# Performance work log

Hardware: AMD Instinct MI355X
Metric: run time of the kernel (lower is better)

The kernel has to match this reference:

```python
import jax, jax.numpy as jnp
import numpy as np

B, T, H, C = 256, 784, 512, 10
TRUNC = 100


def setup_inputs() -> dict:
    key = jax.random.key(0)
    ks = jax.random.split(key, 11)
    s_in = 1.0  # xavier-ish scales
    def init(k, shape, fan_in):
        return jax.random.normal(k, shape, dtype=jnp.float32) * (1.0 / np.sqrt(fan_in))
    return {
        "x": jax.random.normal(ks[0], (B, T), dtype=jnp.float32),
        "W_ih1": init(ks[1], (4 * H, 1), 1),
        "W_hh1": init(ks[2], (4 * H, H), H),
        "b_ih1": jnp.zeros((4 * H,), dtype=jnp.float32),
        "b_hh1": jnp.zeros((4 * H,), dtype=jnp.float32),
        "W_ih2": init(ks[3], (4 * H, H), H),
        "W_hh2": init(ks[4], (4 * H, H), H),
        "b_ih2": jnp.zeros((4 * H,), dtype=jnp.float32),
        "b_hh2": jnp.zeros((4 * H,), dtype=jnp.float32),
        "W_fc": init(ks[5], (C, H), H),
        "b_fc": jnp.zeros((C,), dtype=jnp.float32),
    }


def _lstm_cell(pre, h, c, W_hh, b_hh):
    # pre: input projection [B,4H]; PyTorch LSTMCell gate order: i, f, g, o
    gates = pre + h @ W_hh.T + b_hh
    i, f, g, o = jnp.split(gates, 4, axis=-1)
    c_new = jax.nn.sigmoid(f) * c + jax.nn.sigmoid(i) * jnp.tanh(g)
    h_new = jax.nn.sigmoid(o) * jnp.tanh(c_new)
    return h_new, c_new


def _forward(x, W_ih1, W_hh1, b_ih1, b_hh1, W_ih2, W_hh2, b_ih2, b_hh2, W_fc, b_fc):
    # Precompute input projections for layer 1 across all timesteps: x is scalar per step.
    # pre1_all: [T, B, 4H]
    pre1_all = x.T[:, :, None] * W_ih1[:, 0][None, None, :] + b_ih1
    t_idx = jnp.arange(T)

    def step(carry, xs):
        h1, c1, h2, c2 = carry
        pre1, t = xs
        # truncation point (detach) is identity in forward; kept for structure
        stop = (t % TRUNC) == 0
        sg = lambda a: jnp.where(stop, jax.lax.stop_gradient(a), a)
        h1, c1, h2, c2 = sg(h1), sg(c1), sg(h2), sg(c2)
        h1, c1 = _lstm_cell(pre1, h1, c1, W_hh1, b_hh1)
        pre2 = c1 @ W_ih2.T + b_ih2  # layer 2 consumes layer-1 CELL state
        h2, c2 = _lstm_cell(pre2, h2, c2, W_hh2, b_hh2)
        return (h1, c1, h2, c2), h2

    z = jnp.zeros((B, H), dtype=x.dtype)
    _, outs = jax.lax.scan(step, (z, z, z, z), (pre1_all, t_idx))  # outs: [T,B,H]
    outs = outs.transpose(1, 0, 2)  # [B,T,H]
    out = outs @ W_fc.T + b_fc  # [B,T,C]
    return out


def reference(x, W_ih1, W_hh1, b_ih1, b_hh1, W_ih2, W_hh2, b_ih2, b_hh2, W_fc, b_fc):
    return _forward(x, W_ih1, W_hh1, b_ih1, b_hh1, W_ih2, W_hh2, b_ih2, b_hh2, W_fc, b_fc)
```

## Files before the change

### kernel.cpp

```cpp
#include <hip/hip_runtime.h>


constexpr int Bn = 256;
constexpr int Tn = 784;
constexpr int Hn = 512;
constexpr int Cn = 10;

typedef short s16x8 __attribute__((ext_vector_type(8)));
typedef float f32x4 __attribute__((ext_vector_type(4)));

__device__ __forceinline__ unsigned short f2bf(float f) {
  unsigned u = __float_as_uint(f);
  u += 0x7FFFu + ((u >> 16) & 1u);
  return (unsigned short)(u >> 16);
}
__device__ __forceinline__ float bf2f(unsigned short s) {
  return __uint_as_float(((unsigned)s) << 16);
}
__device__ __forceinline__ float sigm(float v) { return 1.f / (1.f + __expf(-v)); }
__device__ __forceinline__ float tanh_(float v) {
  float vc = fminf(fmaxf(v, -15.f), 15.f);
  float e = __expf(2.f * vc);
  return (e - 1.f) / (e + 1.f);
}

__device__ __forceinline__ s16x8 load16_l2(const unsigned short* p) {
  s16x8 r;
  asm volatile("global_load_dwordx4 %0, %1, off sc0"
               : "=v"(r) : "v"(p) : "memory");
  return r;
}
__device__ __forceinline__ void load16x16_l2(const unsigned short* p, s16x8* f) {
  asm volatile(
      "global_load_dwordx4 %0, %16, off sc0\n\t"
      "global_load_dwordx4 %1, %16, off offset:64 sc0\n\t"
      "global_load_dwordx4 %2, %16, off offset:128 sc0\n\t"
      "global_load_dwordx4 %3, %16, off offset:192 sc0\n\t"
      "global_load_dwordx4 %4, %16, off offset:256 sc0\n\t"
      "global_load_dwordx4 %5, %16, off offset:320 sc0\n\t"
      "global_load_dwordx4 %6, %16, off offset:384 sc0\n\t"
      "global_load_dwordx4 %7, %16, off offset:448 sc0\n\t"
      "global_load_dwordx4 %8, %16, off offset:512 sc0\n\t"
      "global_load_dwordx4 %9, %16, off offset:576 sc0\n\t"
      "global_load_dwordx4 %10, %16, off offset:640 sc0\n\t"
      "global_load_dwordx4 %11, %16, off offset:704 sc0\n\t"
      "global_load_dwordx4 %12, %16, off offset:768 sc0\n\t"
      "global_load_dwordx4 %13, %16, off offset:832 sc0\n\t"
      "global_load_dwordx4 %14, %16, off offset:896 sc0\n\t"
      "global_load_dwordx4 %15, %16, off offset:960 sc0"
      : "=&v"(f[0]), "=&v"(f[1]), "=&v"(f[2]), "=&v"(f[3]),
        "=&v"(f[4]), "=&v"(f[5]), "=&v"(f[6]), "=&v"(f[7]),
        "=&v"(f[8]), "=&v"(f[9]), "=&v"(f[10]), "=&v"(f[11]),
        "=&v"(f[12]), "=&v"(f[13]), "=&v"(f[14]), "=&v"(f[15])
      : "v"(p) : "memory");
}
__device__ __forceinline__ void store4_l2(unsigned short* p, unsigned v0,
                                          unsigned v1, unsigned v2, unsigned v3) {
  asm volatile(
      "global_store_short %0, %1, off\n\t"
      "global_store_short %0, %2, off offset:1024\n\t"
      "global_store_short %0, %3, off offset:2048\n\t"
      "global_store_short %0, %4, off offset:3072"
      :: "v"(p), "v"(v0), "v"(v1), "v"(v2), "v"(v3) : "memory");
}
__device__ __forceinline__ void vm0_fence() {
  asm volatile("s_waitcnt vmcnt(0)" ::: "memory");
  __builtin_amdgcn_sched_barrier(0);
}
__device__ __forceinline__ unsigned ld_flag_mall(const unsigned* p) {
  unsigned r;
  asm volatile("global_load_dword %0, %1, off sc0 sc1\n\ts_waitcnt vmcnt(0)"
               : "=v"(r) : "v"(p) : "memory");
  return r;
}
__device__ __forceinline__ void st_flag_mall(unsigned* p, unsigned v) {
  asm volatile("global_store_dword %0, %1, off sc0 sc1"
               :: "v"(p), "v"(v) : "memory");
}

__device__ __forceinline__ void stage_w(char* smem, const float* W0,
                                        int js, int tid, int base) {
  for (int idx = tid * 4; idx < 64 * 512; idx += 1024) {
    int row = idx >> 9, kk = idx & 511;
    int n = ((row >> 4) << 9) + js + (row & 15);
    float4 w = *(const float4*)(W0 + (size_t)n * Hn + kk);
    short4 v = { (short)f2bf(w.x), (short)f2bf(w.y), (short)f2bf(w.z), (short)f2bf(w.w) };
    int byte = base + (row << 10) + ((((kk >> 3) ^ (row & 7)) << 4)) + ((kk & 7) << 1);
    *(short4*)(smem + byte) = v;
  }
}

__global__ void __launch_bounds__(256, 1)
lstm2_kernel(const float* __restrict__ x,
             const float* __restrict__ W_ih1, const float* __restrict__ W_hh1,
             const float* __restrict__ b_ih1, const float* __restrict__ b_hh1,
             const float* __restrict__ W_ih2, const float* __restrict__ W_hh2,
             const float* __restrict__ b_ih2, const float* __restrict__ b_hh2,
             const float* __restrict__ W_fc, const float* __restrict__ b_fc,
             float* __restrict__ out,
             unsigned* __restrict__ cnts,
             unsigned short* __restrict__ h1b,
             unsigned short* __restrict__ c1b,
             unsigned short* __restrict__ h2b)
{
  extern __shared__ char smem[];
  const int tid = threadIdx.x;
  const int wv = tid >> 6;
  const int l = tid & 63;

  if (tid == 0) {
    unsigned xcc;
    asm volatile("s_getreg_b32 %0, hwreg(HW_REG_XCC_ID)" : "=s"(xcc));
    xcc &= 7u;
    unsigned rk = atomicAdd(&cnts[512 + xcc * 16], 1u);
    *(unsigned*)(smem + 131064) = xcc;
    *(unsigned*)(smem + 131060) = rk;
  }
  __syncthreads();
  const int s8   = (int)*(const unsigned*)(smem + 131064);
  const int rank = (int)(*(const unsigned*)(smem + 131060) & 31u);
  const int rb = s8 << 5;
  const int js = rank << 4;

  unsigned* fbase = cnts + 1024 + s8 * 32;
  unsigned* myflag = fbase + rank;

  const int rA = l & 15, lg = l >> 4, lx = l & 7;
  const bool isW1 = (wv < 2);

  s16x8 bw[64];
  stage_w(smem, W_hh1, js, tid, 0);
  __syncthreads();
  if (isW1) {
#pragma unroll
    for (int g = 0; g < 4; ++g)
#pragma unroll
      for (int kc = 0; kc < 16; ++kc)
        bw[(g << 4) + kc] =
            *(const s16x8*)(smem + (((g << 4) + rA) << 10) + ((((kc << 2) + lg) ^ lx) << 4));
  }
  __syncthreads();
  stage_w(smem, W_hh2, js, tid, 0);
  __syncthreads();
  if (!isW1) {
#pragma unroll
    for (int g = 0; g < 4; ++g)
#pragma unroll
      for (int kc = 0; kc < 16; ++kc)
        bw[(g << 4) + kc] =
            *(const s16x8*)(smem + (((g << 4) + rA) << 10) + ((((kc << 2) + lg) ^ lx) << 4));
  }
  __syncthreads();
  stage_w(smem, W_ih2, js, tid, 0);
  {
    unsigned short* wf = (unsigned short*)(smem + 65536);
    for (int idx = tid; idx < Cn * Hn; idx += 256) wf[idx] = f2bf(W_fc[idx]);
    if (tid < Cn) ((float*)(smem + 65536 + Cn * Hn * 2))[tid] = b_fc[tid];
  }
  __syncthreads();

  float wih1g[4], bg[4];
  {
    int col = js + rA;
#pragma unroll
    for (int g = 0; g < 4; ++g) {
      int n = (g << 9) + col;
      if (isW1) { wih1g[g] = W_ih1[n]; bg[g] = b_ih1[n] + b_hh1[n]; }
      else      { wih1g[g] = 0.f;      bg[g] = b_ih2[n] + b_hh2[n]; }
    }
  }

  const int rf = isW1 ? wv : (wv - 2);
  const int arow  = rb + (rf << 4) + rA;
  const int myrow = rb + (rf << 4) + (lg << 2);
  const int colj = js + rA;
  const int bfc = rb + rank;
  const int cg = wv * 5;

  const size_t SLAB = (size_t)Bn * Hn;
  const size_t aoff = (size_t)arow * Hn + (lg << 3);
  const unsigned short* h1A0 = h1b + aoff;
  const unsigned short* h1A1 = h1b + SLAB + aoff;
  const unsigned short* h2A0 = h2b + aoff;
  const unsigned short* h2A1 = h2b + SLAB + aoff;
  const unsigned short* c1A0 = c1b + aoff;
  const unsigned short* c1A1 = c1b + SLAB + aoff;
  const size_t woff = (size_t)myrow * Hn + colj;
  unsigned short* h1W0 = h1b + woff;  unsigned short* h1W1 = h1b + SLAB + woff;
  unsigned short* c1W0 = c1b + woff;  unsigned short* c1W1 = c1b + SLAB + woff;
  unsigned short* h2W0 = h2b + woff;  unsigned short* h2W1 = h2b + SLAB + woff;
  const unsigned short* fcA0 = h2b + (size_t)bfc * Hn + (l << 3);
  const unsigned short* fcA1 = fcA0 + SLAB;

  float cst[4] = {0.f, 0.f, 0.f, 0.f};

  for (int k = 0; k <= Tn + 1; ++k) {
    if (wv == 0 && k > 0) {
      const unsigned* p = fbase + (l & 31);
      int g = 0;
      for (;;) {
        unsigned a = ld_flag_mall(p);
        if (__all((int)a >= k)) break;
        if (++g > (1 << 20)) break;
        __builtin_amdgcn_s_sleep(1);
      }
    }
    __syncthreads();

    s16x8 h8;
    if (isW1 && k >= 2)
      h8 = load16_l2((k & 1) ? fcA1 : fcA0);

    if (isW1) {
      if (k < Tn) {
        float xv[4];
#pragma unroll
        for (int r = 0; r < 4; ++r) xv[r] = x[(size_t)(myrow + r) * Tn + k];
        s16x8 af[16];
        load16x16_l2(((k - 1) & 1) ? h1A1 : h1A0, af);
        vm0_fence();
        f32x4 acc[4];
#pragma unroll
        for (int g = 0; g < 4; ++g) acc[g] = f32x4{0.f, 0.f, 0.f, 0.f};
#pragma unroll
        for (int kc = 0; kc < 16; ++kc)
#pragma unroll
          for (int g = 0; g < 4; ++g)
            acc[g] = __builtin_amdgcn_mfma_f32_16x16x32_bf16(af[kc], bw[(g << 4) + kc], acc[g], 0, 0, 0);
        unsigned hv[4], cv[4];
#pragma unroll
        for (int r = 0; r < 4; ++r) {
          float iv = sigm(acc[0][r] + xv[r] * wih1g[0] + bg[0]);
          float ff = sigm(acc[1][r] + xv[r] * wih1g[1] + bg[1]);
          float gv = tanh_(acc[2][r] + xv[r] * wih1g[2] + bg[2]);
          float ov = sigm(acc[3][r] + xv[r] * wih1g[3] + bg[3]);
          float c = ff * cst[r] + iv * gv;
          cst[r] = c;
          hv[r] = f2bf(ov * tanh_(c));
          cv[r] = f2bf(c);
        }
        store4_l2((k & 1) ? h1W1 : h1W0, hv[0], hv[1], hv[2], hv[3]);
        store4_l2((k & 1) ? c1W1 : c1W0, cv[0], cv[1], cv[2], cv[3]);
      }
    } else {
      if (k >= 1 && k <= Tn) {
        const int t = k - 1;
        s16x8 af[16], cf[16];
        load16x16_l2(((t - 1) & 1) ? h2A1 : h2A0, af);
        load16x16_l2((t & 1) ? c1A1 : c1A0, cf);
        vm0_fence();
        f32x4 acc[4];
#pragma unroll
        for (int g = 0; g < 4; ++g) acc[g] = f32x4{0.f, 0.f, 0.f, 0.f};
#pragma unroll
        for (int kc = 0; kc < 16; ++kc)
#pragma unroll
          for (int g = 0; g < 4; ++g)
            acc[g] = __builtin_amdgcn_mfma_f32_16x16x32_bf16(af[kc], bw[(g << 4) + kc], acc[g], 0, 0, 0);
#pragma unroll
        for (int kc = 0; kc < 16; ++kc)
#pragma unroll
          for (int g = 0; g < 4; ++g) {
            int byte = (((g << 4) + rA) << 10) + ((((kc << 2) + lg) ^ lx) << 4);
            acc[g] = __builtin_amdgcn_mfma_f32_16x16x32_bf16(cf[kc], *(const s16x8*)(smem + byte), acc[g], 0, 0, 0);
          }
        unsigned hv[4];
#pragma unroll
        for (int r = 0; r < 4; ++r) {
          float iv = sigm(acc[0][r] + bg[0]);
          float ff = sigm(acc[1][r] + bg[1]);
          float gv = tanh_(acc[2][r] + bg[2]);
          float ov = sigm(acc[3][r] + bg[3]);
          float c = ff * cst[r] + iv * gv;
          cst[r] = c;
          hv[r] = f2bf(ov * tanh_(c));
        }
        store4_l2((t & 1) ? h2W1 : h2W0, hv[0], hv[1], hv[2], hv[3]);
      }
    }

    vm0_fence();
    __syncthreads();
    if (tid == 0) st_flag_mall(myflag, (unsigned)(k + 1));

    if (isW1 && k >= 2) {
      const unsigned short* wf = (const unsigned short*)(smem + 65536);
      float rs[5];
#pragma unroll
      for (int c5 = 0; c5 < 5; ++c5) {
        s16x8 w8 = *(const s16x8*)(wf + (size_t)(cg + c5) * Hn + (l << 3));
        float sum = 0.f;
#pragma unroll
        for (int i = 0; i < 8; ++i)
          sum += bf2f((unsigned short)h8[i]) * bf2f((unsigned short)w8[i]);
        rs[c5] = sum;
      }
#pragma unroll
      for (int c5 = 0; c5 < 5; ++c5) {
#pragma unroll
        for (int off = 32; off > 0; off >>= 1)
          rs[c5] += __shfl_xor(rs[c5], off);
      }
      if (l < 5) {
        float v = (l == 0) ? rs[0] : (l == 1) ? rs[1] : (l == 2) ? rs[2] : (l == 3) ? rs[3] : rs[4];
        v += ((const float*)(smem + 65536 + Cn * Hn * 2))[cg + l];
        out[(size_t)bfc * (Tn * Cn) + (size_t)(k - 2) * Cn + (cg + l)] = v;
      }
    }
  }
}

extern "C" void kernel_launch(void* const* d_in, const int* in_sizes, int n_in,
                              void* d_out, int out_size, void* d_ws, size_t ws_size,
                              hipStream_t stream) {
  const float* x     = (const float*)d_in[0];
  const float* W_ih1 = (const float*)d_in[1];
  const float* W_hh1 = (const float*)d_in[2];
  const float* b_ih1 = (const float*)d_in[3];
  const float* b_hh1 = (const float*)d_in[4];
  const float* W_ih2 = (const float*)d_in[5];
  const float* W_hh2 = (const float*)d_in[6];
  const float* b_ih2 = (const float*)d_in[7];
  const float* b_hh2 = (const float*)d_in[8];
  const float* W_fc  = (const float*)d_in[9];
  const float* b_fc  = (const float*)d_in[10];
  float* out = (float*)d_out;

  unsigned* cnts = (unsigned*)d_ws;
  unsigned short* h1b = (unsigned short*)((char*)d_ws + 32768);
  unsigned short* c1b = h1b + (size_t)2 * Bn * Hn;
  unsigned short* h2b = c1b + (size_t)2 * Bn * Hn;

  size_t zbytes = 32768 + (size_t)3 * 2 * Bn * Hn * sizeof(unsigned short);
  hipMemsetAsync(d_ws, 0, zbytes, stream);

  (void)hipFuncSetAttribute((const void*)lstm2_kernel,
                            hipFuncAttributeMaxDynamicSharedMemorySize, 131072);

  lstm2_kernel<<<dim3(256), dim3(256), 131072, stream>>>(
      x, W_ih1, W_hh1, b_ih1, b_hh1, W_ih2, W_hh2, b_ih2, b_hh2, W_fc, b_fc,
      out, cnts, h1b, c1b, h2b);
}
```

Baseline: 4.722 ms.

## Precompute layer-2 input projection one step ahead, off the critical path

Layer-2 workgroups now compute the c1@W_ih2 projection for the next timestep after signalling the step flag, storing it in registers (p2a). The later step only runs the h2@W_hh2 MFMAs before the gate math. The pipeline is deepened to a 4-slot ring for c1, h2 and the FC read, and the loop is extended by two iterations. This shortens the per-step critical path of the grid-wide barrier chain, at the cost of extra workspace, more live registers and two more global synchronisation steps.

```diff
diff --git a/kernel.cpp b/kernel.cpp
--- a/kernel.cpp
+++ b/kernel.cpp
@@ -22,6 +22,10 @@
   float vc = fminf(fmaxf(v, -15.f), 15.f);
   float e = __expf(2.f * vc);
   return (e - 1.f) / (e + 1.f);
+}
+template <typename T>
+__device__ __forceinline__ T sel4(int s, T p0, T p1, T p2, T p3) {
+  return (s == 0) ? p0 : (s == 1) ? p1 : (s == 2) ? p2 : p3;
 }
 
 __device__ __forceinline__ s16x8 load16_l2(const unsigned short* p) {
@@ -179,22 +183,28 @@
 
   const size_t SLAB = (size_t)Bn * Hn;
   const size_t aoff = (size_t)arow * Hn + (lg << 3);
+  const size_t woff = (size_t)myrow * Hn + colj;
   const unsigned short* h1A0 = h1b + aoff;
   const unsigned short* h1A1 = h1b + SLAB + aoff;
-  const unsigned short* h2A0 = h2b + aoff;
-  const unsigned short* h2A1 = h2b + SLAB + aoff;
-  const unsigned short* c1A0 = c1b + aoff;
-  const unsigned short* c1A1 = c1b + SLAB + aoff;
-  const size_t woff = (size_t)myrow * Hn + colj;
   unsigned short* h1W0 = h1b + woff;  unsigned short* h1W1 = h1b + SLAB + woff;
-  unsigned short* c1W0 = c1b + woff;  unsigned short* c1W1 = c1b + SLAB + woff;
-  unsigned short* h2W0 = h2b + woff;  unsigned short* h2W1 = h2b + SLAB + woff;
-  const unsigned short* fcA0 = h2b + (size_t)bfc * Hn + (l << 3);
-  const unsigned short* fcA1 = fcA0 + SLAB;
+  unsigned short* c1W[4] = { c1b + woff, c1b + SLAB + woff,
+                             c1b + 2 * SLAB + woff, c1b + 3 * SLAB + woff };
+  const unsigned short* c1A[4] = { c1b + aoff, c1b + SLAB + aoff,
+                                   c1b + 2 * SLAB + aoff, c1b + 3 * SLAB + aoff };
+  unsigned short* h2W[4] = { h2b + woff, h2b + SLAB + woff,
+                             h2b + 2 * SLAB + woff, h2b + 3 * SLAB + woff };
+  const unsigned short* h2A[4] = { h2b + aoff, h2b + SLAB + aoff,
+                                   h2b + 2 * SLAB + aoff, h2b + 3 * SLAB + aoff };
+  const size_t fcoff = (size_t)bfc * Hn + (l << 3);
+  const unsigned short* fcA[4] = { h2b + fcoff, h2b + SLAB + fcoff,
+                                   h2b + 2 * SLAB + fcoff, h2b + 3 * SLAB + fcoff };
 
   float cst[4] = {0.f, 0.f, 0.f, 0.f};
-
-  for (int k = 0; k <= Tn + 1; ++k) {
+  f32x4 p2a[4];
+#pragma unroll
+  for (int g = 0; g < 4; ++g) p2a[g] = f32x4{0.f, 0.f, 0.f, 0.f};
+
+  for (int k = 0; k <= Tn + 3; ++k) {
     if (wv == 0 && k > 0) {
       const unsigned* p = fbase + (l & 31);
       int g = 0;
@@ -208,8 +218,8 @@
     __syncthreads();
 
     s16x8 h8;
-    if (isW1 && k >= 2)
-      h8 = load16_l2((k & 1) ? fcA1 : fcA0);
+    if (isW1 && k >= 4)
+      h8 = load16_l2(sel4(k & 3, fcA[0], fcA[1], fcA[2], fcA[3]));
 
     if (isW1) {
       if (k < Tn) {
@@ -240,14 +250,13 @@
           cv[r] = f2bf(c);
         }
         store4_l2((k & 1) ? h1W1 : h1W0, hv[0], hv[1], hv[2], hv[3]);
-        store4_l2((k & 1) ? c1W1 : c1W0, cv[0], cv[1], cv[2], cv[3]);
+        store4_l2(sel4(k & 3, c1W[0], c1W[1], c1W[2], c1W[3]), cv[0], cv[1], cv[2], cv[3]);
       }
     } else {
-      if (k >= 1 && k <= Tn) {
-        const int t = k - 1;
-        s16x8 af[16], cf[16];
-        load16x16_l2(((t - 1) & 1) ? h2A1 : h2A0, af);
-        load16x16_l2((t & 1) ? c1A1 : c1A0, cf);
+      if (k >= 2 && k <= Tn + 1) {
+        const int t = k - 2;
+        s16x8 af[16];
+        load16x16_l2(sel4((t - 1) & 3, h2A[0], h2A[1], h2A[2], h2A[3]), af);
         vm0_fence();
         f32x4 acc[4];
 #pragma unroll
@@ -257,25 +266,18 @@
 #pragma unroll
           for (int g = 0; g < 4; ++g)
             acc[g] = __builtin_amdgcn_mfma_f32_16x16x32_bf16(af[kc], bw[(g << 4) + kc], acc[g], 0, 0, 0);
-#pragma unroll
-        for (int kc = 0; kc < 16; ++kc)
-#pragma unroll
-          for (int g = 0; g < 4; ++g) {
-            int byte = (((g << 4) + rA) << 10) + ((((kc << 2) + lg) ^ lx) << 4);
-            acc[g] = __builtin_amdgcn_mfma_f32_16x16x32_bf16(cf[kc], *(const s16x8*)(smem + byte), acc[g], 0, 0, 0);
-          }
         unsigned hv[4];
 #pragma unroll
         for (int r = 0; r < 4; ++r) {
-          float iv = sigm(acc[0][r] + bg[0]);
-          float ff = sigm(acc[1][r] + bg[1]);
-          float gv = tanh_(acc[2][r] + bg[2]);
-          float ov = sigm(acc[3][r] + bg[3]);
+          float iv = sigm(acc[0][r] + p2a[0][r] + bg[0]);
+          float ff = sigm(acc[1][r] + p2a[1][r] + bg[1]);
+          float gv = tanh_(acc[2][r] + p2a[2][r] + bg[2]);
+          float ov = sigm(acc[3][r] + p2a[3][r] + bg[3]);
           float c = ff * cst[r] + iv * gv;
           cst[r] = c;
           hv[r] = f2bf(ov * tanh_(c));
         }
-        store4_l2((t & 1) ? h2W1 : h2W0, hv[0], hv[1], hv[2], hv[3]);
+        store4_l2(sel4(t & 3, h2W[0], h2W[1], h2W[2], h2W[3]), hv[0], hv[1], hv[2], hv[3]);
       }
     }
 
@@ -283,28 +285,45 @@
     __syncthreads();
     if (tid == 0) st_flag_mall(myflag, (unsigned)(k + 1));
 
-    if (isW1 && k >= 2) {
-      const unsigned short* wf = (const unsigned short*)(smem + 65536);
-      float rs[5];
-#pragma unroll
-      for (int c5 = 0; c5 < 5; ++c5) {
-        s16x8 w8 = *(const s16x8*)(wf + (size_t)(cg + c5) * Hn + (l << 3));
-        float sum = 0.f;
-#pragma unroll
-        for (int i = 0; i < 8; ++i)
-          sum += bf2f((unsigned short)h8[i]) * bf2f((unsigned short)w8[i]);
-        rs[c5] = sum;
-      }
-#pragma unroll
-      for (int c5 = 0; c5 < 5; ++c5) {
-#pragma unroll
-        for (int off = 32; off > 0; off >>= 1)
-          rs[c5] += __shfl_xor(rs[c5], off);
-      }
-      if (l < 5) {
-        float v = (l == 0) ? rs[0] : (l == 1) ? rs[1] : (l == 2) ? rs[2] : (l == 3) ? rs[3] : rs[4];
-        v += ((const float*)(smem + 65536 + Cn * Hn * 2))[cg + l];
-        out[(size_t)bfc * (Tn * Cn) + (size_t)(k - 2) * Cn + (cg + l)] = v;
+    if (isW1) {
+      if (k >= 4) {
+        const unsigned short* wf = (const unsigned short*)(smem + 65536);
+        float rs[5];
+#pragma unroll
+        for (int c5 = 0; c5 < 5; ++c5) {
+          s16x8 w8 = *(const s16x8*)(wf + (size_t)(cg + c5) * Hn + (l << 3));
+          float sum = 0.f;
+#pragma unroll
+          for (int i = 0; i < 8; ++i)
+            sum += bf2f((unsigned short)h8[i]) * bf2f((unsigned short)w8[i]);
+          rs[c5] = sum;
+        }
+#pragma unroll
+        for (int c5 = 0; c5 < 5; ++c5) {
+#pragma unroll
+          for (int off = 32; off > 0; off >>= 1)
+            rs[c5] += __shfl_xor(rs[c5], off);
+        }
+        if (l < 5) {
+          float v = (l == 0) ? rs[0] : (l == 1) ? rs[1] : (l == 2) ? rs[2] : (l == 3) ? rs[3] : rs[4];
+          v += ((const float*)(smem + 65536 + Cn * Hn * 2))[cg + l];
+          out[(size_t)bfc * (Tn * Cn) + (size_t)(k - 4) * Cn + (cg + l)] = v;
+        }
+      }
+    } else {
+      if (k >= 1 && k <= Tn) {
+        s16x8 cf[16];
+        load16x16_l2(sel4((k - 1) & 3, c1A[0], c1A[1], c1A[2], c1A[3]), cf);
+        vm0_fence();
+#pragma unroll
+        for (int g = 0; g < 4; ++g) p2a[g] = f32x4{0.f, 0.f, 0.f, 0.f};
+#pragma unroll
+        for (int kc = 0; kc < 16; ++kc)
+#pragma unroll
+          for (int g = 0; g < 4; ++g) {
+            int byte = (((g << 4) + rA) << 10) + ((((kc << 2) + lg) ^ lx) << 4);
+            p2a[g] = __builtin_amdgcn_mfma_f32_16x16x32_bf16(cf[kc], *(const s16x8*)(smem + byte), p2a[g], 0, 0, 0);
+          }
       }
     }
   }
@@ -329,9 +348,9 @@
   unsigned* cnts = (unsigned*)d_ws;
   unsigned short* h1b = (unsigned short*)((char*)d_ws + 32768);
   unsigned short* c1b = h1b + (size_t)2 * Bn * Hn;
-  unsigned short* h2b = c1b + (size_t)2 * Bn * Hn;
-
-  size_t zbytes = 32768 + (size_t)3 * 2 * Bn * Hn * sizeof(unsigned short);
+  unsigned short* h2b = c1b + (size_t)4 * Bn * Hn;
+
+  size_t zbytes = 32768 + (size_t)(2 + 4 + 4) * Bn * Hn * sizeof(unsigned short);
   hipMemsetAsync(d_ws, 0, zbytes, stream);
 
   (void)hipFuncSetAttribute((const void*)lstm2_kernel,
```

Result: slower. 4.955 ms (+4.9%).

## Replace block-level barriers with per-wavefront flags in the inter-block step sync

Applied to the files above, without the earlier changes.

Each wavefront now publishes its own progress flag, padded to 64 bytes, and every wavefront polls all 128 peer flags in the group directly. This lets the two __syncthreads per timestep be removed, and the x loads are hoisted ahead of the spin-wait. The aim is to cut intra-block barrier latency and let wavefronts proceed independently on the serial recurrence critical path. The cost is four times more flag traffic per poll, and correctness now depends on every wavefront's flag covering its own shared-memory and global writes.

```diff
diff --git a/kernel.cpp b/kernel.cpp
--- a/kernel.cpp
+++ b/kernel.cpp
@@ -67,15 +67,17 @@
   asm volatile("s_waitcnt vmcnt(0)" ::: "memory");
   __builtin_amdgcn_sched_barrier(0);
 }
-__device__ __forceinline__ unsigned ld_flag_mall(const unsigned* p) {
-  unsigned r;
-  asm volatile("global_load_dword %0, %1, off sc0 sc1\n\ts_waitcnt vmcnt(0)"
-               : "=v"(r) : "v"(p) : "memory");
-  return r;
-}
 __device__ __forceinline__ void st_flag_mall(unsigned* p, unsigned v) {
   asm volatile("global_store_dword %0, %1, off sc0 sc1"
                :: "v"(p), "v"(v) : "memory");
+}
+__device__ __forceinline__ void ld_flag2_mall(const unsigned* p0,
+                                              const unsigned* p1,
+                                              unsigned& a, unsigned& b) {
+  asm volatile("global_load_dword %0, %2, off sc0 sc1\n\t"
+               "global_load_dword %1, %3, off sc0 sc1\n\t"
+               "s_waitcnt vmcnt(0)"
+               : "=&v"(a), "=&v"(b) : "v"(p0), "v"(p1) : "memory");
 }
 
 __device__ __forceinline__ void stage_w(char* smem, const float* W0,
@@ -122,8 +124,8 @@
   const int rb = s8 << 5;
   const int js = rank << 4;
 
-  unsigned* fbase = cnts + 1024 + s8 * 32;
-  unsigned* myflag = fbase + rank;
+  unsigned* fbase = cnts + 4096 + s8 * 2048;
+  unsigned* myflag = fbase + (((rank << 2) + wv) << 4);
 
   const int rA = l & 15, lg = l >> 4, lx = l & 7;
   const bool isW1 = (wv < 2);
@@ -192,20 +194,29 @@
   const unsigned short* fcA0 = h2b + (size_t)bfc * Hn + (l << 3);
   const unsigned short* fcA1 = fcA0 + SLAB;
 
+  const unsigned* pf0 = fbase + (l << 4);
+  const unsigned* pf1 = pf0 + 1024;
+
   float cst[4] = {0.f, 0.f, 0.f, 0.f};
 
   for (int k = 0; k <= Tn + 1; ++k) {
-    if (wv == 0 && k > 0) {
-      const unsigned* p = fbase + (l & 31);
+    float xv[4];
+    const bool doL1 = isW1 && (k < Tn);
+    if (doL1) {
+#pragma unroll
+      for (int r = 0; r < 4; ++r) xv[r] = x[(size_t)(myrow + r) * Tn + k];
+    }
+
+    if (k > 0) {
       int g = 0;
       for (;;) {
-        unsigned a = ld_flag_mall(p);
-        if (__all((int)a >= k)) break;
+        unsigned a, b;
+        ld_flag2_mall(pf0, pf1, a, b);
+        if (__all((int)a >= k && (int)b >= k)) break;
         if (++g > (1 << 20)) break;
         __builtin_amdgcn_s_sleep(1);
       }
     }
-    __syncthreads();
 
     s16x8 h8;
     if (isW1 && k >= 2)
@@ -213,9 +224,6 @@
 
     if (isW1) {
       if (k < Tn) {
-        float xv[4];
-#pragma unroll
-        for (int r = 0; r < 4; ++r) xv[r] = x[(size_t)(myrow + r) * Tn + k];
         s16x8 af[16];
         load16x16_l2(((k - 1) & 1) ? h1A1 : h1A0, af);
         vm0_fence();
@@ -280,8 +288,7 @@
     }
 
     vm0_fence();
-    __syncthreads();
-    if (tid == 0) st_flag_mall(myflag, (unsigned)(k + 1));
+    if (l == 0) st_flag_mall(myflag, (unsigned)(k + 1));
 
     if (isW1 && k >= 2) {
       const unsigned short* wf = (const unsigned short*)(smem + 65536);
@@ -327,11 +334,11 @@
   float* out = (float*)d_out;
 
   unsigned* cnts = (unsigned*)d_ws;
-  unsigned short* h1b = (unsigned short*)((char*)d_ws + 32768);
+  unsigned short* h1b = (unsigned short*)((char*)d_ws + 131072);
   unsigned short* c1b = h1b + (size_t)2 * Bn * Hn;
   unsigned short* h2b = c1b + (size_t)2 * Bn * Hn;
 
-  size_t zbytes = 32768 + (size_t)3 * 2 * Bn * Hn * sizeof(unsigned short);
+  size_t zbytes = 131072 + (size_t)3 * 2 * Bn * Hn * sizeof(unsigned short);
   hipMemsetAsync(d_ws, 0, zbytes, stream);
 
   (void)hipFuncSetAttribute((const void*)lstm2_kernel,
```

Result: slower. 5.855 ms (+24.0%).
